# Performance work log

Hardware: AMD Instinct MI355X
Metric: run time of the kernel (lower is better)

## Reference

```python
import jax, jax.numpy as jnp
import numpy as np

BSZ, N, F_IN, H, D = 8, 20000, 256, 8, 64
E = 160000  # flattened edge-slot count per batch row (includes head multiplicity)


def setup_inputs() -> dict:
    key = jax.random.key(0)
    k1, k2, k3, k4, k5, k6 = jax.random.split(key, 6)
    concept_hidden = jax.random.normal(k1, (BSZ, N, F_IN), dtype=jnp.float32)
    head = jax.random.randint(k2, (BSZ, E), 0, BSZ * N * H, dtype=jnp.int64)
    tail = jax.random.randint(k3, (BSZ, E), 0, BSZ * N * H, dtype=jnp.int64)
    W_proj = jax.random.normal(k4, (H * D, F_IN), dtype=jnp.float32) * 0.05
    scoring_src = jax.random.normal(k5, (BSZ, 1, H, D), dtype=jnp.float32) * 0.05
    scoring_trg = jax.random.normal(k6, (BSZ, 1, H, D), dtype=jnp.float32) * 0.05
    return {"concept_hidden": concept_hidden, "head": head, "tail": tail,
            "W_proj": W_proj, "scoring_src": scoring_src, "scoring_trg": scoring_trg}


def reference(concept_hidden, head, tail, W_proj, scoring_src, scoring_trg):
    bsz = concept_hidden.shape[0]
    # linear_proj (no bias): [bsz, N, F_in] @ W^T -> [bsz, N, H*D] -> [bsz, N, H, D]
    proj = jnp.einsum('bnf,of->bno', concept_hidden, W_proj)
    proj = proj.reshape(bsz, -1, H, D)
    # broadcast mul + sum over feature dim -> per-node, per-head scores [bsz, N, H]
    scores_source = jnp.einsum('bnhd,bohd->bnh', proj, scoring_src)
    scores_target = jnp.einsum('bnhd,bohd->bnh', proj, scoring_trg)
    # lift: gather from globally-flattened [bsz*N*H] score vector
    ss = scores_source.reshape(-1)[head.reshape(-1)].reshape(bsz, -1)
    st = scores_target.reshape(-1)[tail.reshape(-1)].reshape(bsz, -1)
    return jax.nn.sigmoid(ss + st)
```

## Files before the change

kernel.cpp:

```cpp
#include <hip/hip_runtime.h>
#include <math.h>

#define BSZ 8
#define NN 20000
#define F_IN 256
#define H 8
#define D 64
#define E 160000

typedef _Float16 half_t;
typedef float  fx4 __attribute__((ext_vector_type(4)));
typedef int    ix4 __attribute__((ext_vector_type(4)));

__global__ __launch_bounds__(256) void fold_weights(
        const float* __restrict__ W_proj,
        const float* __restrict__ s_src,
        const float* __restrict__ s_trg,
        float* __restrict__ w_src,
        float* __restrict__ w_trg) {
    __shared__ float ls[D];
    __shared__ float lt[D];
    const int b = blockIdx.x >> 3;
    const int h = blockIdx.x & 7;
    const int f = threadIdx.x;
    if (threadIdx.x < D) {
        ls[threadIdx.x] = s_src[((size_t)b * H + h) * D + threadIdx.x];
        lt[threadIdx.x] = s_trg[((size_t)b * H + h) * D + threadIdx.x];
    }
    __syncthreads();
    float as = 0.f, at = 0.f;
#pragma unroll 8
    for (int d = 0; d < D; ++d) {
        const float wp = W_proj[((size_t)(h * D + d)) * F_IN + f];
        as = fmaf(wp, ls[d], as);
        at = fmaf(wp, lt[d], at);
    }
    w_src[((size_t)b * H + h) * F_IN + f] = as;
    w_trg[((size_t)b * H + h) * F_IN + f] = at;
}

#define RPAD 260
__global__ __launch_bounds__(256) void node_scores(
        const float* __restrict__ ch,
        const float* __restrict__ w_src,
        const float* __restrict__ w_trg,
        half_t* __restrict__ sc_src,
        half_t* __restrict__ sc_trg) {
    __shared__ float lws[H][RPAD];
    __shared__ float lwt[H][RPAD];
    __shared__ float rows[32][RPAD];

    const int bx = blockIdx.x;
    const int b = bx / 625;
    const int tile = bx % 625;

    const float* gws = w_src + (size_t)b * H * F_IN;
    const float* gwt = w_trg + (size_t)b * H * F_IN;
    for (int i = threadIdx.x; i < H * F_IN; i += 256) {
        lws[i >> 8][i & 255] = gws[i];
        lwt[i >> 8][i & 255] = gwt[i];
    }

    const fx4* __restrict__ g4 =
        (const fx4*)(ch + ((size_t)b * NN + (size_t)tile * 32) * F_IN);
#pragma unroll 8
    for (int i = threadIdx.x; i < 32 * (F_IN / 4); i += 256) {
        const int r = i >> 6;
        const int c = i & 63;
        *((fx4*)&rows[r][c * 4]) = __builtin_nontemporal_load(&g4[i]);
    }
    __syncthreads();

    const int h = threadIdx.x & 7;
    const int nl = threadIdx.x >> 3;
    const int n = tile * 32 + nl;

    const fx4* __restrict__ crow = (const fx4*)(&rows[nl][0]);
    const fx4* __restrict__ wsr  = (const fx4*)(&lws[h][0]);
    const fx4* __restrict__ wtr  = (const fx4*)(&lwt[h][0]);

    float as = 0.f, at = 0.f;
#pragma unroll 8
    for (int f4 = 0; f4 < F_IN / 4; ++f4) {
        const fx4 c = crow[f4];
        const fx4 s = wsr[f4];
        const fx4 t = wtr[f4];
        as = fmaf(c.x, s.x, as); as = fmaf(c.y, s.y, as);
        as = fmaf(c.z, s.z, as); as = fmaf(c.w, s.w, as);
        at = fmaf(c.x, t.x, at); at = fmaf(c.y, t.y, at);
        at = fmaf(c.z, t.z, at); at = fmaf(c.w, t.w, at);
    }

    const size_t oi = ((size_t)b * NN + n) * H + h;
    sc_src[oi] = (half_t)as;
    sc_trg[oi] = (half_t)at;
}

__global__ __launch_bounds__(256) void gather_sigmoid(
        const ix4* __restrict__ head4,
        const ix4* __restrict__ tail4,
        const half_t* __restrict__ sc_src,
        const half_t* __restrict__ sc_trg,
        fx4* __restrict__ out4, int total4) {
    const int i = blockIdx.x * 256 + threadIdx.x;
    if (i < total4) {
        const ix4 hh = __builtin_nontemporal_load(&head4[i]);
        const ix4 tt = __builtin_nontemporal_load(&tail4[i]);
        fx4 r;
        r.x = (float)sc_src[hh.x] + (float)sc_trg[tt.x];
        r.y = (float)sc_src[hh.y] + (float)sc_trg[tt.y];
        r.z = (float)sc_src[hh.z] + (float)sc_trg[tt.z];
        r.w = (float)sc_src[hh.w] + (float)sc_trg[tt.w];
        r.x = 1.f / (1.f + __expf(-r.x));
        r.y = 1.f / (1.f + __expf(-r.y));
        r.z = 1.f / (1.f + __expf(-r.z));
        r.w = 1.f / (1.f + __expf(-r.w));
        __builtin_nontemporal_store(r, &out4[i]);
    }
}

extern "C" void kernel_launch(void* const* d_in, const int* in_sizes, int n_in,
                              void* d_out, int out_size, void* d_ws, size_t ws_size,
                              hipStream_t stream) {
    const float* ch   = (const float*)d_in[0];
    const int*   head = (const int*)d_in[1];
    const int*   tail = (const int*)d_in[2];
    const float* W    = (const float*)d_in[3];
    const float* ssrc = (const float*)d_in[4];
    const float* strg = (const float*)d_in[5];
    float* out = (float*)d_out;

    float* ws = (float*)d_ws;
    float* w_src  = ws;
    float* w_trg  = ws + BSZ * H * F_IN;
    half_t* sc_src = (half_t*)(ws + 2 * BSZ * H * F_IN);
    half_t* sc_trg = sc_src + (size_t)BSZ * NN * H;

    fold_weights<<<BSZ * H, 256, 0, stream>>>(W, ssrc, strg, w_src, w_trg);
    node_scores<<<BSZ * 625, 256, 0, stream>>>(ch, w_src, w_trg, sc_src, sc_trg);
    const int total4 = (BSZ * E) / 4;
    gather_sigmoid<<<(total4 + 255) / 256, 256, 0, stream>>>(
        (const ix4*)head, (const ix4*)tail, sc_src, sc_trg, (fx4*)out, total4);
}
```

Baseline: 278.7 us.

## Read node rows directly from global memory, two rows per thread group

The node_scores kernel no longer stages a 32-row tile of concept_hidden in shared memory. Each 8-thread group now handles two rows, which it reads straight from global memory with nontemporal vector loads and accumulates in vector registers. Blocks cover 64 rows, halving the grid, and launch bounds request two blocks per CU. This removes the LDS staging and its bandwidth, at the cost of 8 threads (one per head) loading the same row addresses and relying on cache coalescing for that reuse.

```diff
diff --git a/kernel.cpp b/kernel.cpp
--- a/kernel.cpp
+++ b/kernel.cpp
@@ -40,7 +40,10 @@
 }
 
 #define RPAD 260
-__global__ __launch_bounds__(256) void node_scores(
+#define TILE_ROWS 64
+#define NT_TILES 313
+
+__global__ __launch_bounds__(256, 2) void node_scores(
         const float* __restrict__ ch,
         const float* __restrict__ w_src,
         const float* __restrict__ w_trg,
@@ -48,11 +51,9 @@
         half_t* __restrict__ sc_trg) {
     __shared__ float lws[H][RPAD];
     __shared__ float lwt[H][RPAD];
-    __shared__ float rows[32][RPAD];
 
-    const int bx = blockIdx.x;
-    const int b = bx / 625;
-    const int tile = bx % 625;
+    const int b = blockIdx.x / NT_TILES;
+    const int tile = blockIdx.x % NT_TILES;
 
     const float* gws = w_src + (size_t)b * H * F_IN;
     const float* gwt = w_trg + (size_t)b * H * F_IN;
@@ -60,40 +61,50 @@
         lws[i >> 8][i & 255] = gws[i];
         lwt[i >> 8][i & 255] = gwt[i];
     }
-
-    const fx4* __restrict__ g4 =
-        (const fx4*)(ch + ((size_t)b * NN + (size_t)tile * 32) * F_IN);
-#pragma unroll 8
-    for (int i = threadIdx.x; i < 32 * (F_IN / 4); i += 256) {
-        const int r = i >> 6;
-        const int c = i & 63;
-        *((fx4*)&rows[r][c * 4]) = __builtin_nontemporal_load(&g4[i]);
-    }
     __syncthreads();
 
     const int h = threadIdx.x & 7;
-    const int nl = threadIdx.x >> 3;
-    const int n = tile * 32 + nl;
+    const int g = threadIdx.x >> 3;
+    const int row0 = tile * TILE_ROWS + g * 2;
+    const int row1 = row0 + 1;
+    const int r0c = row0 < NN ? row0 : NN - 1;
+    const int r1c = row1 < NN ? row1 : NN - 1;
 
-    const fx4* __restrict__ crow = (const fx4*)(&rows[nl][0]);
-    const fx4* __restrict__ wsr  = (const fx4*)(&lws[h][0]);
-    const fx4* __restrict__ wtr  = (const fx4*)(&lwt[h][0]);
+    const fx4* __restrict__ rp0 = (const fx4*)(ch + ((size_t)b * NN + r0c) * F_IN);
+    const fx4* __restrict__ rp1 = (const fx4*)(ch + ((size_t)b * NN + r1c) * F_IN);
+    const fx4* __restrict__ ws4 = (const fx4*)(&lws[h][0]);
+    const fx4* __restrict__ wt4 = (const fx4*)(&lwt[h][0]);
 
-    float as = 0.f, at = 0.f;
-#pragma unroll 8
+    fx4 a0s = {0.f, 0.f, 0.f, 0.f}, a0t = {0.f, 0.f, 0.f, 0.f};
+    fx4 a1s = {0.f, 0.f, 0.f, 0.f}, a1t = {0.f, 0.f, 0.f, 0.f};
+
+#pragma unroll 4
     for (int f4 = 0; f4 < F_IN / 4; ++f4) {
-        const fx4 c = crow[f4];
-        const fx4 s = wsr[f4];
-        const fx4 t = wtr[f4];
-        as = fmaf(c.x, s.x, as); as = fmaf(c.y, s.y, as);
-        as = fmaf(c.z, s.z, as); as = fmaf(c.w, s.w, as);
-        at = fmaf(c.x, t.x, at); at = fmaf(c.y, t.y, at);
-        at = fmaf(c.z, t.z, at); at = fmaf(c.w, t.w, at);
+        const fx4 s = ws4[f4];
+        const fx4 t = wt4[f4];
+        const fx4 c0 = __builtin_nontemporal_load(&rp0[f4]);
+        const fx4 c1 = __builtin_nontemporal_load(&rp1[f4]);
+        a0s += c0 * s;
+        a0t += c0 * t;
+        a1s += c1 * s;
+        a1t += c1 * t;
     }
 
-    const size_t oi = ((size_t)b * NN + n) * H + h;
-    sc_src[oi] = (half_t)as;
-    sc_trg[oi] = (half_t)at;
+    const float s0 = (a0s.x + a0s.y) + (a0s.z + a0s.w);
+    const float t0 = (a0t.x + a0t.y) + (a0t.z + a0t.w);
+    const float s1 = (a1s.x + a1s.y) + (a1s.z + a1s.w);
+    const float t1 = (a1t.x + a1t.y) + (a1t.z + a1t.w);
+
+    if (row0 < NN) {
+        const size_t oi = ((size_t)b * NN + row0) * H + h;
+        sc_src[oi] = (half_t)s0;
+        sc_trg[oi] = (half_t)t0;
+    }
+    if (row1 < NN) {
+        const size_t oi = ((size_t)b * NN + row1) * H + h;
+        sc_src[oi] = (half_t)s1;
+        sc_trg[oi] = (half_t)t1;
+    }
 }
 
 __global__ __launch_bounds__(256) void gather_sigmoid(
@@ -137,7 +148,7 @@
     half_t* sc_trg = sc_src + (size_t)BSZ * NN * H;
 
     fold_weights<<<BSZ * H, 256, 0, stream>>>(W, ssrc, strg, w_src, w_trg);
-    node_scores<<<BSZ * 625, 256, 0, stream>>>(ch, w_src, w_trg, sc_src, sc_trg);
+    node_scores<<<BSZ * NT_TILES, 256, 0, stream>>>(ch, w_src, w_trg, sc_src, sc_trg);
     const int total4 = (BSZ * E) / 4;
     gather_sigmoid<<<(total4 + 255) / 256, 256, 0, stream>>>(
         (const ix4*)head, (const ix4*)tail, sc_src, sc_trg, (fx4*)out, total4);
```

Measured after the change: 320.8 us. +15.1%, slower.

## Compute node scores with fp16 MFMA using per-wave swizzled LDS tiles

Applied to the files above, without the earlier changes.

Rewrites node_scores so each wave loads a 16-row tile of concept_hidden, converts it to fp16 in swizzled LDS, and runs 16x16x32 f16 MFMA against the folded src/trg weights, which are now stored as fp16 in a 16-column layout. This replaces the scalar FMA dot products and the block-wide shared weight staging and barrier. The input read of about 164MB dominates, so the gain depends on whether the kernel was compute- or latency-bound. The fp16 rounding of the inputs and weights reduces accuracy.

```diff
diff --git a/kernel.cpp b/kernel.cpp
--- a/kernel.cpp
+++ b/kernel.cpp
@@ -11,13 +11,14 @@
 typedef _Float16 half_t;
 typedef float  fx4 __attribute__((ext_vector_type(4)));
 typedef int    ix4 __attribute__((ext_vector_type(4)));
+typedef _Float16 hx8 __attribute__((ext_vector_type(8)));
+typedef _Float16 hx4 __attribute__((ext_vector_type(4)));
 
 __global__ __launch_bounds__(256) void fold_weights(
         const float* __restrict__ W_proj,
         const float* __restrict__ s_src,
         const float* __restrict__ s_trg,
-        float* __restrict__ w_src,
-        float* __restrict__ w_trg) {
+        half_t* __restrict__ w16) {
     __shared__ float ls[D];
     __shared__ float lt[D];
     const int b = blockIdx.x >> 3;
@@ -35,65 +36,68 @@
         as = fmaf(wp, ls[d], as);
         at = fmaf(wp, lt[d], at);
     }
-    w_src[((size_t)b * H + h) * F_IN + f] = as;
-    w_trg[((size_t)b * H + h) * F_IN + f] = at;
+    w16[((size_t)b * 16 + h) * F_IN + f]     = (half_t)as;
+    w16[((size_t)b * 16 + 8 + h) * F_IN + f] = (half_t)at;
 }
 
-#define RPAD 260
+#define TROWS 16
+#define TILES_PER_B (NN / TROWS)
+#define TOTAL_TILES (BSZ * TILES_PER_B)
+
 __global__ __launch_bounds__(256) void node_scores(
         const float* __restrict__ ch,
-        const float* __restrict__ w_src,
-        const float* __restrict__ w_trg,
+        const half_t* __restrict__ w16,
         half_t* __restrict__ sc_src,
         half_t* __restrict__ sc_trg) {
-    __shared__ float lws[H][RPAD];
-    __shared__ float lwt[H][RPAD];
-    __shared__ float rows[32][RPAD];
+    __shared__ _Float16 lds_all[4][TROWS * F_IN];
 
-    const int bx = blockIdx.x;
-    const int b = bx / 625;
-    const int tile = bx % 625;
+    const int wave = threadIdx.x >> 6;
+    const int lane = threadIdx.x & 63;
+    const int tile = blockIdx.x * 4 + wave;
+    const int b    = tile / TILES_PER_B;
+    const int row0 = (tile % TILES_PER_B) * TROWS;
 
-    const float* gws = w_src + (size_t)b * H * F_IN;
-    const float* gwt = w_trg + (size_t)b * H * F_IN;
-    for (int i = threadIdx.x; i < H * F_IN; i += 256) {
-        lws[i >> 8][i & 255] = gws[i];
-        lwt[i >> 8][i & 255] = gwt[i];
+    char* lbase = (char*)&lds_all[wave][0];
+
+    const int n    = lane & 15;
+    const int kgrp = lane >> 4;
+
+    hx8 bf[8];
+    {
+        const half_t* wb = w16 + ((size_t)b * 16 + n) * F_IN + kgrp * 8;
+#pragma unroll
+        for (int s = 0; s < 8; ++s)
+            bf[s] = *(const hx8*)(wb + s * 32);
     }
 
-    const fx4* __restrict__ g4 =
-        (const fx4*)(ch + ((size_t)b * NN + (size_t)tile * 32) * F_IN);
-#pragma unroll 8
-    for (int i = threadIdx.x; i < 32 * (F_IN / 4); i += 256) {
-        const int r = i >> 6;
-        const int c = i & 63;
-        *((fx4*)&rows[r][c * 4]) = __builtin_nontemporal_load(&g4[i]);
-    }
-    __syncthreads();
-
-    const int h = threadIdx.x & 7;
-    const int nl = threadIdx.x >> 3;
-    const int n = tile * 32 + nl;
-
-    const fx4* __restrict__ crow = (const fx4*)(&rows[nl][0]);
-    const fx4* __restrict__ wsr  = (const fx4*)(&lws[h][0]);
-    const fx4* __restrict__ wtr  = (const fx4*)(&lwt[h][0]);
-
-    float as = 0.f, at = 0.f;
-#pragma unroll 8
-    for (int f4 = 0; f4 < F_IN / 4; ++f4) {
-        const fx4 c = crow[f4];
-        const fx4 s = wsr[f4];
-        const fx4 t = wtr[f4];
-        as = fmaf(c.x, s.x, as); as = fmaf(c.y, s.y, as);
-        as = fmaf(c.z, s.z, as); as = fmaf(c.w, s.w, as);
-        at = fmaf(c.x, t.x, at); at = fmaf(c.y, t.y, at);
-        at = fmaf(c.z, t.z, at); at = fmaf(c.w, t.w, at);
+    const float* gsrc = ch + ((size_t)b * NN + row0) * F_IN;
+#pragma unroll
+    for (int i = 0; i < TROWS; ++i) {
+        const fx4 v = __builtin_nontemporal_load(
+            (const fx4*)(gsrc + (size_t)i * F_IN) + lane);
+        hx4 h4;
+        h4.x = (half_t)v.x; h4.y = (half_t)v.y;
+        h4.z = (half_t)v.z; h4.w = (half_t)v.w;
+        const int off = (i * 512 + lane * 8) ^ ((i & 7) << 4);
+        *(hx4*)(lbase + off) = h4;
     }
 
-    const size_t oi = ((size_t)b * NN + n) * H + h;
-    sc_src[oi] = (half_t)as;
-    sc_trg[oi] = (half_t)at;
+    fx4 acc = {0.f, 0.f, 0.f, 0.f};
+#pragma unroll
+    for (int s = 0; s < 8; ++s) {
+        const int off = ((lane & 15) * 512 + s * 64 + kgrp * 16)
+                        ^ ((lane & 7) << 4);
+        const hx8 af = *(const hx8*)(lbase + off);
+        acc = __builtin_amdgcn_mfma_f32_16x16x32_f16(af, bf[s], acc, 0, 0, 0);
+    }
+
+#pragma unroll
+    for (int r = 0; r < 4; ++r) {
+        const int row = row0 + kgrp * 4 + r;
+        const half_t val = (half_t)acc[r];
+        if (n < 8) sc_src[((size_t)b * NN + row) * H + n]       = val;
+        else       sc_trg[((size_t)b * NN + row) * H + (n - 8)] = val;
+    }
 }
 
 __global__ __launch_bounds__(256) void gather_sigmoid(
@@ -130,14 +134,13 @@
     const float* strg = (const float*)d_in[5];
     float* out = (float*)d_out;
 
-    float* ws = (float*)d_ws;
-    float* w_src  = ws;
-    float* w_trg  = ws + BSZ * H * F_IN;
-    half_t* sc_src = (half_t*)(ws + 2 * BSZ * H * F_IN);
+    char* base = (char*)d_ws;
+    half_t* w16    = (half_t*)base;
+    half_t* sc_src = (half_t*)(base + 65536);
     half_t* sc_trg = sc_src + (size_t)BSZ * NN * H;
 
-    fold_weights<<<BSZ * H, 256, 0, stream>>>(W, ssrc, strg, w_src, w_trg);
-    node_scores<<<BSZ * 625, 256, 0, stream>>>(ch, w_src, w_trg, sc_src, sc_trg);
+    fold_weights<<<BSZ * H, 256, 0, stream>>>(W, ssrc, strg, w16);
+    node_scores<<<TOTAL_TILES / 4, 256, 0, stream>>>(ch, w16, sc_src, sc_trg);
     const int total4 = (BSZ * E) / 4;
     gather_sigmoid<<<(total4 + 255) / 256, 256, 0, stream>>>(
         (const ix4*)head, (const ix4*)tail, sc_src, sc_trg, (fx4*)out, total4);
```

New measurement: 250.2 us. -10.2%, faster.
